# Optimization experiments

Measured on AMD Instinct MI355X. Metric: run time of the kernel, lower is better.

Reference implementation:

```python
import jax, jax.numpy as jnp
import numpy as np

N = 16384   # total gate nodes (64 graphs x 256 gates)
B = 64      # graphs in batch
E = 49152   # directed edges (avg in-degree 3)
Q = 32      # qubit_num
F = 256     # feat_dim
D = 2 * F   # node feature dim = 512
H = 2       # heads
A = 128     # action_num


def _gatv2(x, wl, wr, att, b, src, dst, n):
    # PyG GATv2Conv (concat=True, share_weights=False, negative_slope=0.2)
    h, c = att.shape
    xl = (x @ wl).reshape(n, h, c)   # source-side projection [N,H,C]
    xr = (x @ wr).reshape(n, h, c)   # target-side projection [N,H,C]
    e = jax.nn.leaky_relu(xl[src] + xr[dst], 0.2)       # [E,H,C]
    logit = jnp.einsum('ehc,hc->eh', e, att)             # [E,H]
    m = jax.ops.segment_max(logit, dst, num_segments=n)  # softmax over in-edges per target
    p = jnp.exp(logit - m[dst])
    den = jax.ops.segment_sum(p, dst, num_segments=n)
    alpha = p / den[dst]                                 # [E,H]
    out = jax.ops.segment_sum(alpha[:, :, None] * xl[src], dst, num_segments=n)
    return out.reshape(n, h * c) + b


def _forward(x, xt_w1, xt_b1, xt_w2, xt_b2,
             g0_wl, g0_wr, g0_att, g0_b,
             g1_wl, g1_wr, g1_att, g1_b,
             g2_wl, g2_wr, g2_att, g2_b,
             g3_wl, g3_wr, g3_att, g3_b,
             g4_wl, g4_wr, g4_att, g4_b,
             ln_w, ln_b, aggr_t,
             m_w1, m_b1, m_w2, m_b2, m_w3, m_b3,
             edge_index, batch):
    lr = lambda v: jax.nn.leaky_relu(v, 0.01)
    # x_trans: Linear -> LeakyReLU -> Linear, then fold qubit-pairs into one node
    h0 = lr(x @ xt_w1 + xt_b1) @ xt_w2 + xt_b2           # [2N, F]
    cx = h0.reshape(-1, D)                               # [N, 2F]
    n = cx.shape[0]
    # GATv2Conv default add_self_loops=True (inputs contain no self loops)
    sl = jnp.arange(n, dtype=edge_index.dtype)
    src = jnp.concatenate([edge_index[0], sl])
    dst = jnp.concatenate([edge_index[1], sl])
    res = cx
    h = lr(_gatv2(cx, g0_wl, g0_wr, g0_att, g0_b, src, dst, n))
    for wl_, wr_, att_, b_ in ((g1_wl, g1_wr, g1_att, g1_b),
                               (g2_wl, g2_wr, g2_att, g2_b),
                               (g3_wl, g3_wr, g3_att, g3_b)):
        h = lr(_gatv2(h, wl_, wr_, att_, b_, src, dst, n))
    h = lr(_gatv2(h, g4_wl, g4_wr, g4_att, g4_b, src, dst, n))
    h = h + res                                           # residual [N, 2F]
    # PyG LayerNorm(mode='graph'): normalize over nodes AND channels per graph
    cnt = jax.ops.segment_sum(jnp.ones((n,), h.dtype), batch, num_segments=B)
    norm = cnt * h.shape[1]
    mean = jax.ops.segment_sum(h.sum(-1), batch, num_segments=B) / norm
    hc = h - mean[batch][:, None]
    var = jax.ops.segment_sum((hc * hc).sum(-1), batch, num_segments=B) / norm
    h = hc / jnp.sqrt(var + 1e-5)[batch][:, None] * ln_w + ln_b
    # SoftmaxAggregation(learn=True): channel-wise softmax over nodes per graph
    logit = h * aggr_t
    mg = jax.ops.segment_max(logit, batch, num_segments=B)
    p = jnp.exp(logit - mg[batch])
    den = jax.ops.segment_sum(p, batch, num_segments=B)
    g = jax.ops.segment_sum((p / den[batch]) * h, batch, num_segments=B)  # [B, 2F]
    # head MLP 512->384->256->128
    o = lr(g @ m_w1 + m_b1)
    o = lr(o @ m_w2 + m_b2)
    return o @ m_w3 + m_b3


def setup_inputs() -> dict:
    key = jax.random.key(0)
    ks = iter(jax.random.split(key, 64))
    def rn(shp, s=0.05):
        return jax.random.normal(next(ks), shp, jnp.float32) * s
    d = {}
    d['x'] = jax.random.normal(next(ks), (2 * N, Q), jnp.float32)
    src = jax.random.randint(next(ks), (E,), 0, N, jnp.int32)
    off = jax.random.randint(next(ks), (E,), 1, N, jnp.int32)
    d['edge_index'] = jnp.stack([src, (src + off) % N])  # no self loops
    d['batch'] = jnp.arange(N, dtype=jnp.int32) // (N // B)
    d['xt_w1'] = rn((Q, F)); d['xt_b1'] = rn((F,))
    d['xt_w2'] = rn((F, F)); d['xt_b2'] = rn((F,))
    d['g0_wl'] = rn((D, H * D)); d['g0_wr'] = rn((D, H * D))
    d['g0_att'] = rn((H, D));    d['g0_b'] = rn((H * D,))
    for i in (1, 2, 3):
        d[f'g{i}_wl'] = rn((H * D, H * D)); d[f'g{i}_wr'] = rn((H * D, H * D))
        d[f'g{i}_att'] = rn((H, D));        d[f'g{i}_b'] = rn((H * D,))
    d['g4_wl'] = rn((H * D, D)); d['g4_wr'] = rn((H * D, D))
    d['g4_att'] = rn((1, D));    d['g4_b'] = rn((D,))
    d['ln_w'] = jnp.ones((D,), jnp.float32); d['ln_b'] = jnp.zeros((D,), jnp.float32)
    d['aggr_t'] = jnp.array(1.0, jnp.float32)
    d['m_w1'] = rn((D, 384)); d['m_b1'] = rn((384,))
    d['m_w2'] = rn((384, 256)); d['m_b2'] = rn((256,))
    d['m_w3'] = rn((256, A)); d['m_b3'] = rn((A,))
    return d


def reference(x, edge_index, batch, xt_w1, xt_b1, xt_w2, xt_b2,
              g0_wl, g0_wr, g0_att, g0_b,
              g1_wl, g1_wr, g1_att, g1_b,
              g2_wl, g2_wr, g2_att, g2_b,
              g3_wl, g3_wr, g3_att, g3_b,
              g4_wl, g4_wr, g4_att, g4_b,
              ln_w, ln_b, aggr_t,
              m_w1, m_b1, m_w2, m_b2, m_w3, m_b3):
    return _forward(x, xt_w1, xt_b1, xt_w2, xt_b2,
                    g0_wl, g0_wr, g0_att, g0_b,
                    g1_wl, g1_wr, g1_att, g1_b,
                    g2_wl, g2_wr, g2_att, g2_b,
                    g3_wl, g3_wr, g3_att, g3_b,
                    g4_wl, g4_wr, g4_att, g4_b,
                    ln_w, ln_b, aggr_t,
                    m_w1, m_b1, m_w2, m_b2, m_w3, m_b3,
                    edge_index, batch)
```

## Files before the change

kernel.cpp:

```cpp
#include <hip/hip_runtime.h>
#include <hip/hip_bf16.h>

typedef __hip_bfloat16 bf16;

#define NN 16384
#define BBG 64
#define EE 49152
#define ET (EE + NN)
#define DD 512
#define NG (NN / BBG)

__device__ __forceinline__ float b2f(bf16 v) { return __bfloat162float(v); }
__device__ __forceinline__ bf16 f2b(float v) { return __float2bfloat16(v); }
__device__ __forceinline__ float sb2f(short s) {
    unsigned u = ((unsigned)(unsigned short)s) << 16;
    return __builtin_bit_cast(float, u);
}
__device__ __forceinline__ short f2bs(float v) {
    bf16 b = f2b(v);
    return __builtin_bit_cast(short, b);
}
__device__ __forceinline__ int clampi(int v, int lo, int hi)
{
    return v < lo ? lo : (v > hi ? hi : v);
}

typedef __attribute__((ext_vector_type(8))) short bf16x8;
typedef __attribute__((ext_vector_type(4))) float f32x4;

#define AS1 __attribute__((address_space(1)))
#define AS3 __attribute__((address_space(3)))

__global__ __launch_bounds__(256) void gemm_mfma_bt(
    const bf16* __restrict__ A, const bf16* __restrict__ Bt,
    const float* __restrict__ bias, float* __restrict__ C,
    bf16* __restrict__ Cb, int M, int N, int K, float slope, int has_act)
{
    __shared__ bf16 As[128 * 32];
    __shared__ bf16 Bs[128 * 32];
    const int tid = threadIdx.x;
    const int w = tid >> 6;
    const int l = tid & 63;
    const int bm = blockIdx.y * 128;
    const int bn = blockIdx.x * 128;
    const int wrow = (w >> 1) * 64;
    const int wcol = (w & 1) * 64;
    const int quad = l >> 4;
    const int c16 = l & 15;

    const int lrow = l >> 2;
    const int lchunk = l & 3;
    const bf16* Ag = A + (size_t)(bm + w * 16 + lrow) * K + lchunk * 8;
    const bf16* Bg = Bt + (size_t)(bn + w * 16 + lrow) * K + lchunk * 8;
    char* AsB = (char*)As;
    char* BsB = (char*)Bs;

    f32x4 acc[4][4] = {};

    for (int k0 = 0; k0 < K; k0 += 32) {
        __builtin_amdgcn_global_load_lds((const AS1 void*)(Ag + k0),
            (AS3 void*)(AsB + w * 1024), 16, 0, 0);
        __builtin_amdgcn_global_load_lds((const AS1 void*)(Ag + (size_t)64 * K + k0),
            (AS3 void*)(AsB + 4096 + w * 1024), 16, 0, 0);
        __builtin_amdgcn_global_load_lds((const AS1 void*)(Bg + k0),
            (AS3 void*)(BsB + w * 1024), 16, 0, 0);
        __builtin_amdgcn_global_load_lds((const AS1 void*)(Bg + (size_t)64 * K + k0),
            (AS3 void*)(BsB + 4096 + w * 1024), 16, 0, 0);
        __syncthreads();

        bf16x8 a[4], b[4];
#pragma unroll
        for (int i = 0; i < 4; i++) {
            int ra = wrow + i * 16 + c16;
            a[i] = *(const bf16x8*)(AsB + ra * 64 + quad * 16);
            int rb = wcol + i * 16 + c16;
            b[i] = *(const bf16x8*)(BsB + rb * 64 + quad * 16);
        }
#pragma unroll
        for (int i = 0; i < 4; i++)
#pragma unroll
            for (int j = 0; j < 4; j++)
                acc[i][j] = __builtin_amdgcn_mfma_f32_16x16x32_bf16(
                    a[i], b[j], acc[i][j], 0, 0, 0);
        __syncthreads();
    }

#pragma unroll
    for (int i = 0; i < 4; i++) {
#pragma unroll
        for (int j = 0; j < 4; j++) {
            int col = bn + wcol + j * 16 + c16;
            float bv = bias ? bias[col] : 0.f;
#pragma unroll
            for (int r = 0; r < 4; r++) {
                int row = bm + wrow + i * 16 + quad * 4 + r;
                float v = acc[i][j][r] + bv;
                if (has_act) v = (v >= 0.f) ? v : v * slope;
                if (C)  C[(size_t)row * N + col] = v;
                if (Cb) Cb[(size_t)row * N + col] = f2b(v);
            }
        }
    }
}

__global__ __launch_bounds__(256) void gemm_mfma_dual(
    const bf16* __restrict__ A, const bf16* __restrict__ Bt,
    bf16* __restrict__ X0, bf16* __restrict__ X1,
    int M, int Ntot, int K, int HC)
{
    __shared__ bf16 As[128 * 32];
    __shared__ bf16 Bs[128 * 32];
    const int tid = threadIdx.x;
    const int w = tid >> 6;
    const int l = tid & 63;
    const int bm = blockIdx.y * 128;
    const int bn = blockIdx.x * 128;
    const int wrow = (w >> 1) * 64;
    const int wcol = (w & 1) * 64;
    const int quad = l >> 4;
    const int c16 = l & 15;

    const int lrow = l >> 2;
    const int lchunk = l & 3;
    const bf16* Ag = A + (size_t)(bm + w * 16 + lrow) * K + lchunk * 8;
    const bf16* Bg = Bt + (size_t)(bn + w * 16 + lrow) * K + lchunk * 8;
    char* AsB = (char*)As;
    char* BsB = (char*)Bs;

    f32x4 acc[4][4] = {};

    for (int k0 = 0; k0 < K; k0 += 32) {
        __builtin_amdgcn_global_load_lds((const AS1 void*)(Ag + k0),
            (AS3 void*)(AsB + w * 1024), 16, 0, 0);
        __builtin_amdgcn_global_load_lds((const AS1 void*)(Ag + (size_t)64 * K + k0),
            (AS3 void*)(AsB + 4096 + w * 1024), 16, 0, 0);
        __builtin_amdgcn_global_load_lds((const AS1 void*)(Bg + k0),
            (AS3 void*)(BsB + w * 1024), 16, 0, 0);
        __builtin_amdgcn_global_load_lds((const AS1 void*)(Bg + (size_t)64 * K + k0),
            (AS3 void*)(BsB + 4096 + w * 1024), 16, 0, 0);
        __syncthreads();

        bf16x8 a[4], b[4];
#pragma unroll
        for (int i = 0; i < 4; i++) {
            int ra = wrow + i * 16 + c16;
            a[i] = *(const bf16x8*)(AsB + ra * 64 + quad * 16);
            int rb = wcol + i * 16 + c16;
            b[i] = *(const bf16x8*)(BsB + rb * 64 + quad * 16);
        }
#pragma unroll
        for (int i = 0; i < 4; i++)
#pragma unroll
            for (int j = 0; j < 4; j++)
                acc[i][j] = __builtin_amdgcn_mfma_f32_16x16x32_bf16(
                    a[i], b[j], acc[i][j], 0, 0, 0);
        __syncthreads();
    }

#pragma unroll
    for (int i = 0; i < 4; i++) {
#pragma unroll
        for (int j = 0; j < 4; j++) {
            int col = bn + wcol + j * 16 + c16;
            bf16* dst = (col < HC) ? (X0 + col) : (X1 + col - HC);
#pragma unroll
            for (int r = 0; r < 4; r++) {
                int row = bm + wrow + i * 16 + quad * 4 + r;
                dst[(size_t)row * HC] = f2b(acc[i][j][r]);
            }
        }
    }
}

__global__ __launch_bounds__(256) void gemm_f32(
    const float* __restrict__ A, const float* __restrict__ W,
    const float* __restrict__ bias, float* __restrict__ C,
    int M, int N, int K, float slope, int has_act)
{
    const int BK = 16;
    __shared__ float Asm[BK][64 + 1];
    __shared__ float Wsm[BK][64 + 1];
    int tid = threadIdx.x;
    int bm = blockIdx.y * 64;
    int bn = blockIdx.x * 64;
    int tr = tid >> 4;
    int tc = tid & 15;
    float acc[4][4] = {};

    for (int k0 = 0; k0 < K; k0 += BK) {
        {
            int col = tid & 15;
            int row = tid >> 4;
#pragma unroll
            for (int p = 0; p < 4; p++) {
                int r = row + p * 16;
                Asm[col][r] = A[(size_t)(bm + r) * K + k0 + col];
            }
        }
        {
            int wc = tid & 63;
            int wr = tid >> 6;
#pragma unroll
            for (int p = 0; p < 4; p++) {
                int r = wr + p * 4;
                Wsm[r][wc] = W[(size_t)(k0 + r) * N + bn + wc];
            }
        }
        __syncthreads();
#pragma unroll
        for (int kk = 0; kk < BK; kk++) {
            float a[4], w[4];
#pragma unroll
            for (int i = 0; i < 4; i++) a[i] = Asm[kk][tr * 4 + i];
#pragma unroll
            for (int j = 0; j < 4; j++) w[j] = Wsm[kk][tc * 4 + j];
#pragma unroll
            for (int i = 0; i < 4; i++)
#pragma unroll
                for (int j = 0; j < 4; j++)
                    acc[i][j] += a[i] * w[j];
        }
        __syncthreads();
    }
#pragma unroll
    for (int i = 0; i < 4; i++) {
        int r = bm + tr * 4 + i;
#pragma unroll
        for (int j = 0; j < 4; j++) {
            int cn = bn + tc * 4 + j;
            float v = acc[i][j];
            if (bias) v += bias[cn];
            if (has_act) v = (v >= 0.f) ? v : v * slope;
            C[(size_t)r * N + cn] = v;
        }
    }
}

__global__ __launch_bounds__(256) void transpose_f2b2(
    const float* __restrict__ in0, bf16* __restrict__ out0,
    const float* __restrict__ in1, bf16* __restrict__ out1, int R, int C)
{
    const float* in = blockIdx.z ? in1 : in0;
    bf16* out = blockIdx.z ? out1 : out0;
    __shared__ float tile[32][33];
    int c0 = blockIdx.x * 32;
    int r0 = blockIdx.y * 32;
    int tx = threadIdx.x & 31;
    int ty = threadIdx.x >> 5;
#pragma unroll
    for (int k = 0; k < 4; k++) {
        int r = ty + k * 8;
        tile[r][tx] = in[(size_t)(r0 + r) * C + c0 + tx];
    }
    __syncthreads();
#pragma unroll
    for (int k = 0; k < 4; k++) {
        int rr = ty + k * 8;
        out[(size_t)(c0 + rr) * R + r0 + tx] = f2b(tile[tx][rr]);
    }
}

__global__ void f2b_vec(const float* __restrict__ in, bf16* __restrict__ out, int n)
{
    int i = blockIdx.x * 256 + threadIdx.x;
    if (i < n) out[i] = f2b(in[i]);
}

__global__ void count_deg(const int* __restrict__ ei, int* __restrict__ deg)
{
    int e = blockIdx.x * 256 + threadIdx.x;
    if (e >= ET) return;
    int d = (e < EE) ? ei[EE + e] : (e - EE);
    d = clampi(d, 0, NN - 1);
    atomicAdd(&deg[d], 1);
}

__global__ __launch_bounds__(256) void scan_deg(const int* __restrict__ deg,
                                                int* __restrict__ rs)
{
    __shared__ int part[256];
    __shared__ int psum[257];
    int tid = threadIdx.x;
    const int per = NN / 256;
    int base = tid * per;
    int s = 0;
    for (int i = 0; i < per; i++) s += deg[base + i];
    part[tid] = s;
    __syncthreads();
    if (tid == 0) {
        int acc = 0;
        for (int i = 0; i < 256; i++) { psum[i] = acc; acc += part[i]; }
        psum[256] = acc;
    }
    __syncthreads();
    int acc = psum[tid];
    for (int i = 0; i < per; i++) { rs[base + i] = acc; acc += deg[base + i]; }
    if (tid == 0) rs[NN] = psum[256];
}

__global__ void fill_csr(const int* __restrict__ ei, const int* __restrict__ rs,
                         int* __restrict__ cur, int* __restrict__ csrc)
{
    int e = blockIdx.x * 256 + threadIdx.x;
    if (e >= ET) return;
    int s, d;
    if (e < EE) { s = ei[e]; d = ei[EE + e]; } else { s = d = e - EE; }
    s = clampi(s, 0, NN - 1);
    d = clampi(d, 0, NN - 1);
    int pos = atomicAdd(&cur[d], 1);
    int slot = clampi(rs[d] + pos, 0, ET - 1);
    csrc[slot] = s;
}

template<int NH>
__global__ __launch_bounds__(256, 4) void gat_wave4(
    const bf16* __restrict__ xl, const bf16* __restrict__ xr,
    const float* __restrict__ att, const float* __restrict__ bias,
    const int* __restrict__ rs, const int* __restrict__ csrc,
    const float* __restrict__ res, float* __restrict__ out_f,
    bf16* __restrict__ out_b, float* __restrict__ lnsums)
{
    constexpr int HC = NH * 512;
    constexpr int PF = 8;
    const int tid = threadIdx.x;
    const int w = tid >> 6;
    const int lane = tid & 63;
    const int gw = blockIdx.x * 4 + w;
    const int n  = (NH == 2) ? (gw >> 1) : gw;
    const int h  = (NH == 2) ? (gw & 1) : 0;
    const int cb = h * 512 + lane * 8;

    int start = rs[n];
    int deg = clampi(rs[n + 1] - start, 1, 64);
    start = clampi(start, 0, ET - 1);
    start = __builtin_amdgcn_readfirstlane(start);
    deg = __builtin_amdgcn_readfirstlane(deg);
    const int dm1 = deg - 1;
    int my_src = csrc[start + ((lane < deg) ? lane : dm1)];
    my_src = clampi(my_src, 0, NN - 1);

    f32x4 rpx = *(const f32x4*)(xr + (size_t)n * HC + cb);
    f32x4 a0 = *(const f32x4*)(att + cb);
    f32x4 a1 = *(const f32x4*)(att + cb + 4);
    f32x4 rows[PF];
#pragma unroll
    for (int r = 0; r < PF; r++) {
        int s = __shfl(my_src, (r < dm1) ? r : dm1);
        rows[r] = *(const f32x4*)(xl + (size_t)s * HC + cb);
    }
    asm volatile("" : "+v"(rpx), "+v"(rows[0]), "+v"(rows[1]), "+v"(rows[2]),
                      "+v"(rows[3]), "+v"(rows[4]), "+v"(rows[5]),
                      "+v"(rows[6]), "+v"(rows[7]));

    float rv[8], av[8];
    {
        bf16x8 xb = __builtin_bit_cast(bf16x8, rpx);
#pragma unroll
        for (int k = 0; k < 8; k++) rv[k] = sb2f(xb[k]);
#pragma unroll
        for (int k = 0; k < 4; k++) { av[k] = a0[k]; av[4 + k] = a1[k]; }
    }

    float part[PF];
#pragma unroll
    for (int r = 0; r < PF; r++) {
        bf16x8 rb = __builtin_bit_cast(bf16x8, rows[r]);
        float p0 = 0.f, p1 = 0.f, p2 = 0.f, p3 = 0.f;
#pragma unroll
        for (int k = 0; k < 8; k += 4) {
            float x0 = sb2f(rb[k + 0]);
            float x1 = sb2f(rb[k + 1]);
            float x2 = sb2f(rb[k + 2]);
            float x3 = sb2f(rb[k + 3]);
            float u0 = x0 + rv[k + 0]; u0 = (u0 >= 0.f) ? u0 : 0.2f * u0;
            float u1 = x1 + rv[k + 1]; u1 = (u1 >= 0.f) ? u1 : 0.2f * u1;
            float u2 = x2 + rv[k + 2]; u2 = (u2 >= 0.f) ? u2 : 0.2f * u2;
            float u3 = x3 + rv[k + 3]; u3 = (u3 >= 0.f) ? u3 : 0.2f * u3;
            p0 = fmaf(av[k + 0], u0, p0);
            p1 = fmaf(av[k + 1], u1, p1);
            p2 = fmaf(av[k + 2], u2, p2);
            p3 = fmaf(av[k + 3], u3, p3);
        }
        part[r] = (p0 + p1) + (p2 + p3);
    }

#pragma unroll
    for (int msk = 32; msk; msk >>= 1) {
#pragma unroll
        for (int r = 0; r < PF; r++) part[r] += __shfl_xor(part[r], msk);
    }

    float m = -1e30f;
#pragma unroll
    for (int r = 0; r < PF; r++) {
        float vr = (r < deg) ? part[r] : -1e30f;
        m = fmaxf(m, vr);
    }
    float den = 0.f;
    float pw[PF];
#pragma unroll
    for (int r = 0; r < PF; r++) {
        float e = __expf(part[r] - m);
        pw[r] = (r < deg) ? e : 0.f;
        den += pw[r];
    }

    float acc[8];
#pragma unroll
    for (int k = 0; k < 8; k++) acc[k] = 0.f;
#pragma unroll
    for (int r = 0; r < PF; r++) {
        bf16x8 rb = __builtin_bit_cast(bf16x8, rows[r]);
#pragma unroll
        for (int k = 0; k < 8; k++)
            acc[k] = fmaf(pw[r], sb2f(rb[k]), acc[k]);
    }

    if (deg > PF) {
        for (int i = PF; i < deg; i++) {
            int s = __shfl(my_src, i);
            f32x4 rw = *(const f32x4*)(xl + (size_t)s * HC + cb);
            bf16x8 rb = __builtin_bit_cast(bf16x8, rw);
            float pt = 0.f;
#pragma unroll
            for (int k = 0; k < 8; k++) {
                float x = sb2f(rb[k]);
                float u = x + rv[k];
                u = (u >= 0.f) ? u : 0.2f * u;
                pt = fmaf(av[k], u, pt);
            }
#pragma unroll
            for (int msk = 32; msk; msk >>= 1) pt += __shfl_xor(pt, msk);
            float mn = fmaxf(m, pt);
            float rr = __expf(m - mn);
            float pi = __expf(pt - mn);
            m = mn;
            den = den * rr + pi;
#pragma unroll
            for (int k = 0; k < 8; k++) {
                float x = sb2f(rb[k]);
                acc[k] = fmaf(acc[k], rr, pi * x);
            }
        }
    }

    float inv = 1.f / den;
    f32x4 b0 = *(const f32x4*)(bias + cb);
    f32x4 b1 = *(const f32x4*)(bias + cb + 4);
    float ls = 0.f, ls2 = 0.f;
    float vals[8];
#pragma unroll
    for (int k = 0; k < 8; k++) {
        float bv = (k < 4) ? b0[k] : b1[k - 4];
        float v = fmaf(acc[k], inv, bv);
        v = (v >= 0.f) ? v : 0.01f * v;
        vals[k] = v;
    }
    if (res) {
#pragma unroll
        for (int k = 0; k < 8; k++) {
            vals[k] += res[(size_t)n * HC + cb + k];
            ls += vals[k];
            ls2 += vals[k] * vals[k];
        }
#pragma unroll
        for (int v = 0; v < 2; v++) {
            f32x4 ov;
#pragma unroll
            for (int k = 0; k < 4; k++) ov[k] = vals[v * 4 + k];
            *(f32x4*)(out_f + (size_t)n * HC + cb + v * 4) = ov;
        }
    } else {
        bf16x8 ov;
#pragma unroll
        for (int k = 0; k < 8; k++) ov[k] = f2bs(vals[k]);
        *(bf16x8*)(out_b + (size_t)n * HC + cb) = ov;
    }

    if (lnsums) {
#pragma unroll
        for (int msk = 32; msk; msk >>= 1) {
            ls += __shfl_xor(ls, msk);
            ls2 += __shfl_xor(ls2, msk);
        }
        if (lane == 0) {
            int g = n >> 8;
            atomicAdd(&lnsums[g], ls);
            atomicAdd(&lnsums[BBG + g], ls2);
        }
    }
}

__global__ __launch_bounds__(256) void aggr_partial(
    const float* __restrict__ h, const float* __restrict__ lnsums,
    const float* __restrict__ lnw, const float* __restrict__ lnb,
    const float* __restrict__ t_, float* __restrict__ pm,
    float* __restrict__ pd, float* __restrict__ pa)
{
    int g = blockIdx.x, ch = blockIdx.y, nk = blockIdx.z;
    int tid = threadIdx.x;
    int c = ch * 256 + tid;
    const float tot = (float)(NG * DD);
    float S = lnsums[g], S2 = lnsums[BBG + g];
    float mu = S / tot;
    float iv = rsqrtf(fmaxf(S2 / tot - mu * mu, 0.f) + 1e-5f);
    float w = lnw[c], b = lnb[c], t = t_[0];
    size_t base = (size_t)g * NG * DD + (size_t)nk * 32 * DD + c;
    float m = -1e30f, den = 0.f, acc = 0.f;
    for (int i = 0; i < 32; i++) {
        float hn = (h[base + (size_t)i * DD] - mu) * iv * w + b;
        float lg = hn * t;
        if (lg > m) {
            float r = __expf(m - lg);
            den *= r; acc *= r; m = lg;
        }
        float p = __expf(lg - m);
        den += p; acc += p * hn;
    }
    size_t idx = (((size_t)g * 2 + ch) * 8 + nk) * 256 + tid;
    pm[idx] = m; pd[idx] = den; pa[idx] = acc;
}

__global__ __launch_bounds__(256) void aggr_combine(
    const float* __restrict__ pm, const float* __restrict__ pd,
    const float* __restrict__ pa, float* __restrict__ gout)
{
    int g = blockIdx.x, ch = blockIdx.y;
    int tid = threadIdx.x;
    size_t base = (((size_t)g * 2 + ch) * 8) * 256 + tid;
    float m = -1e30f;
#pragma unroll
    for (int k = 0; k < 8; k++) m = fmaxf(m, pm[base + k * 256]);
    float den = 0.f, acc = 0.f;
#pragma unroll
    for (int k = 0; k < 8; k++) {
        float r = __expf(pm[base + k * 256] - m);
        den += pd[base + k * 256] * r;
        acc += pa[base + k * 256] * r;
    }
    gout[(size_t)g * DD + ch * 256 + tid] = acc / den;
}

extern "C" void kernel_launch(void* const* d_in, const int* in_sizes, int n_in,
                              void* d_out, int out_size, void* d_ws, size_t ws_size,
                              hipStream_t stream)
{
    const float* x      = (const float*)d_in[0];
    const int*   ei     = (const int*)d_in[1];
    const float* xt_w1  = (const float*)d_in[3];
    const float* xt_b1  = (const float*)d_in[4];
    const float* xt_w2  = (const float*)d_in[5];
    const float* xt_b2  = (const float*)d_in[6];
    const float* ln_w   = (const float*)d_in[27];
    const float* ln_b   = (const float*)d_in[28];
    const float* aggr_t = (const float*)d_in[29];
    const float* m_w1   = (const float*)d_in[30];
    const float* m_b1   = (const float*)d_in[31];
    const float* m_w2   = (const float*)d_in[32];
    const float* m_b2   = (const float*)d_in[33];
    const float* m_w3   = (const float*)d_in[34];
    const float* m_b3   = (const float*)d_in[35];
    float* out = (float*)d_out;

    char* p = (char*)d_ws;
    auto take = [&](size_t bytes) {
        char* r = p;
        p += (bytes + 255) & ~(size_t)255;
        return r;
    };
    int* i_deg     = (int*)take((size_t)(NN + 1) * 4);
    int* i_rs      = (int*)take((size_t)(NN + 1) * 4);
    int* i_cur     = (int*)take((size_t)NN * 4);
    int* i_src     = (int*)take((size_t)ET * 4);
    float* f_sums  = (float*)take((size_t)2 * BBG * 4);
    float* f_pm    = (float*)take((size_t)BBG * 2 * 8 * 256 * 4);
    float* f_pd    = (float*)take((size_t)BBG * 2 * 8 * 256 * 4);
    float* f_pa    = (float*)take((size_t)BBG * 2 * 8 * 256 * 4);
    float* b_g     = (float*)take((size_t)BBG * DD * 4);
    float* b_m1    = (float*)take((size_t)BBG * 384 * 4);
    float* b_m2    = (float*)take((size_t)BBG * 256 * 4);
    float* b_res   = (float*)take((size_t)NN * DD * 4);
    float* b_h     = (float*)take((size_t)NN * DD * 4);
    bf16* b_resb   = (bf16*)take((size_t)NN * DD * 2);
    bf16* b_hb     = (bf16*)take((size_t)NN * 1024 * 2);
    bf16* b_xlb    = (bf16*)take((size_t)NN * 1024 * 2);
    bf16* b_xrb    = (bf16*)take((size_t)NN * 1024 * 2);
    bf16* b_xb     = (bf16*)take((size_t)2 * NN * 32 * 2);
    bf16* b_wcat   = (bf16*)take((size_t)2048 * 1024 * 2);
    bf16* b_w1b    = (bf16*)take((size_t)32 * 256 * 2);
    bf16* b_w2b    = (bf16*)take((size_t)256 * 256 * 2);
    bf16* b_t1b = b_hb;

    dim3 blk(256);

    hipMemsetAsync(i_deg, 0, (size_t)(NN + 1) * 4, stream);
    hipMemsetAsync(i_cur, 0, (size_t)NN * 4, stream);
    hipMemsetAsync(f_sums, 0, (size_t)2 * BBG * 4, stream);
    count_deg<<<ET / 256, blk, 0, stream>>>(ei, i_deg);
    scan_deg<<<1, blk, 0, stream>>>(i_deg, i_rs);
    fill_csr<<<ET / 256, blk, 0, stream>>>(ei, i_rs, i_cur, i_src);

    f2b_vec<<<(2 * NN * 32 + 255) / 256, blk, 0, stream>>>(x, b_xb, 2 * NN * 32);
    transpose_f2b2<<<dim3(256 / 32, 32 / 32, 1), blk, 0, stream>>>(
        xt_w1, b_w1b, xt_w1, b_w1b, 32, 256);
    transpose_f2b2<<<dim3(256 / 32, 256 / 32, 1), blk, 0, stream>>>(
        xt_w2, b_w2b, xt_w2, b_w2b, 256, 256);

    gemm_mfma_bt<<<dim3(256 / 128, 32768 / 128), blk, 0, stream>>>(
        b_xb, b_w1b, xt_b1, (float*)nullptr, b_t1b, 32768, 256, 32, 0.01f, 1);
    gemm_mfma_bt<<<dim3(256 / 128, 32768 / 128), blk, 0, stream>>>(
        b_t1b, b_w2b, xt_b2, b_res, b_resb, 32768, 256, 256, 0.f, 0);

    for (int L = 0; L < 5; L++) {
        const float* wl  = (const float*)d_in[7 + 4 * L];
        const float* wr  = (const float*)d_in[8 + 4 * L];
        const float* att = (const float*)d_in[9 + 4 * L];
        const float* gb  = (const float*)d_in[10 + 4 * L];
        int Fin = (L == 0) ? 512 : 1024;
        int HC  = (L == 4) ? 512 : 1024;
        const bf16* hin = (L == 0) ? b_resb : b_hb;

        transpose_f2b2<<<dim3(HC / 32, Fin / 32, 2), blk, 0, stream>>>(
            wl, b_wcat, wr, b_wcat + (size_t)HC * Fin, Fin, HC);
        gemm_mfma_dual<<<dim3(2 * HC / 128, NN / 128), blk, 0, stream>>>(
            hin, b_wcat, b_xlb, b_xrb, NN, 2 * HC, Fin, HC);
        if (L == 4) {
            gat_wave4<1><<<NN / 4, blk, 0, stream>>>(
                b_xlb, b_xrb, att, gb, i_rs, i_src,
                b_res, b_h, (bf16*)nullptr, f_sums);
        } else {
            gat_wave4<2><<<NN * 2 / 4, blk, 0, stream>>>(
                b_xlb, b_xrb, att, gb, i_rs, i_src,
                (const float*)nullptr, (float*)nullptr, b_hb, (float*)nullptr);
        }
    }

    aggr_partial<<<dim3(BBG, 2, 8), blk, 0, stream>>>(
        b_h, f_sums, ln_w, ln_b, aggr_t, f_pm, f_pd, f_pa);
    aggr_combine<<<dim3(BBG, 2), blk, 0, stream>>>(f_pm, f_pd, f_pa, b_g);

    gemm_f32<<<dim3(384 / 64, 1), blk, 0, stream>>>(
        b_g, m_w1, m_b1, b_m1, 64, 384, 512, 0.01f, 1);
    gemm_f32<<<dim3(256 / 64, 1), blk, 0, stream>>>(
        b_m1, m_w2, m_b2, b_m2, 64, 256, 384, 0.01f, 1);
    gemm_f32<<<dim3(128 / 64, 1), blk, 0, stream>>>(
        b_m2, m_w3, m_b3, out, 64, 128, 256, 0.f, 0);
}
```

Baseline: 1.091 ms.

## Process several nodes per wave with double-buffered neighbor row prefetch

The GAT aggregation kernel now assigns 8 (two-head) or 4 (single-head) node-head tasks to each wave and launches a fixed 1024 blocks. It preloads CSR source indices for all tasks and double-buffers the gathered neighbor rows, so the loads for the next task are in flight while the current one is computed. The number of eagerly prefetched rows drops from 8 to 6 to make room for the second buffer. The aim is to hide gather latency. In exchange, register pressure rises, there are fewer waves in total, and nodes with more than 6 in-edges take the slower serial path more often.

Measured after the change: 1.116 ms. 1.02x slower.

```diff
diff --git a/kernel.cpp b/kernel.cpp
--- a/kernel.cpp
+++ b/kernel.cpp
@@ -313,7 +313,7 @@
 }
 
 template<int NH>
-__global__ __launch_bounds__(256, 4) void gat_wave4(
+__global__ __launch_bounds__(256, 4) void gat_wave5(
     const bf16* __restrict__ xl, const bf16* __restrict__ xr,
     const float* __restrict__ att, const float* __restrict__ bias,
     const int* __restrict__ rs, const int* __restrict__ csrc,
@@ -321,173 +321,234 @@
     bf16* __restrict__ out_b, float* __restrict__ lnsums)
 {
     constexpr int HC = NH * 512;
-    constexpr int PF = 8;
+    constexpr int PF = 6;
+    constexpr int NODES = (NH == 2) ? 8 : 4;
     const int tid = threadIdx.x;
     const int w = tid >> 6;
     const int lane = tid & 63;
-    const int gw = blockIdx.x * 4 + w;
-    const int n  = (NH == 2) ? (gw >> 1) : gw;
-    const int h  = (NH == 2) ? (gw & 1) : 0;
-    const int cb = h * 512 + lane * 8;
-
-    int start = rs[n];
-    int deg = clampi(rs[n + 1] - start, 1, 64);
-    start = clampi(start, 0, ET - 1);
-    start = __builtin_amdgcn_readfirstlane(start);
-    deg = __builtin_amdgcn_readfirstlane(deg);
-    const int dm1 = deg - 1;
-    int my_src = csrc[start + ((lane < deg) ? lane : dm1)];
-    my_src = clampi(my_src, 0, NN - 1);
-
-    f32x4 rpx = *(const f32x4*)(xr + (size_t)n * HC + cb);
-    f32x4 a0 = *(const f32x4*)(att + cb);
-    f32x4 a1 = *(const f32x4*)(att + cb + 4);
-    f32x4 rows[PF];
-#pragma unroll
-    for (int r = 0; r < PF; r++) {
-        int s = __shfl(my_src, (r < dm1) ? r : dm1);
-        rows[r] = *(const f32x4*)(xl + (size_t)s * HC + cb);
-    }
-    asm volatile("" : "+v"(rpx), "+v"(rows[0]), "+v"(rows[1]), "+v"(rows[2]),
-                      "+v"(rows[3]), "+v"(rows[4]), "+v"(rows[5]),
-                      "+v"(rows[6]), "+v"(rows[7]));
-
-    float rv[8], av[8];
+    const int wave_id = blockIdx.x * 4 + w;
+
+    int msrc[NODES];
+    int sdeg[NODES];
+#pragma unroll
+    for (int it = 0; it < NODES; ++it) {
+        int gw = wave_id * NODES + it;
+        int n = (NH == 2) ? (gw >> 1) : gw;
+        int st = rs[n];
+        int deg = clampi(rs[n + 1] - st, 1, 64);
+        st = clampi(st, 0, ET - 1);
+        st = __builtin_amdgcn_readfirstlane(st);
+        deg = __builtin_amdgcn_readfirstlane(deg);
+        sdeg[it] = deg;
+        msrc[it] = csrc[st + ((lane < deg) ? lane : deg - 1)];
+    }
+    if (NH == 2) {
+        asm volatile("" : "+v"(msrc[0]), "+v"(msrc[1]), "+v"(msrc[2]),
+                          "+v"(msrc[3]), "+v"(msrc[4]), "+v"(msrc[5]),
+                          "+v"(msrc[6]), "+v"(msrc[7]));
+    } else {
+        asm volatile("" : "+v"(msrc[0]), "+v"(msrc[1]), "+v"(msrc[2]),
+                          "+v"(msrc[3]));
+    }
+
+    float av0[8], av1[8];
     {
-        bf16x8 xb = __builtin_bit_cast(bf16x8, rpx);
-#pragma unroll
-        for (int k = 0; k < 8; k++) rv[k] = sb2f(xb[k]);
-#pragma unroll
-        for (int k = 0; k < 4; k++) { av[k] = a0[k]; av[4 + k] = a1[k]; }
-    }
-
-    float part[PF];
-#pragma unroll
-    for (int r = 0; r < PF; r++) {
-        bf16x8 rb = __builtin_bit_cast(bf16x8, rows[r]);
-        float p0 = 0.f, p1 = 0.f, p2 = 0.f, p3 = 0.f;
-#pragma unroll
-        for (int k = 0; k < 8; k += 4) {
-            float x0 = sb2f(rb[k + 0]);
-            float x1 = sb2f(rb[k + 1]);
-            float x2 = sb2f(rb[k + 2]);
-            float x3 = sb2f(rb[k + 3]);
-            float u0 = x0 + rv[k + 0]; u0 = (u0 >= 0.f) ? u0 : 0.2f * u0;
-            float u1 = x1 + rv[k + 1]; u1 = (u1 >= 0.f) ? u1 : 0.2f * u1;
-            float u2 = x2 + rv[k + 2]; u2 = (u2 >= 0.f) ? u2 : 0.2f * u2;
-            float u3 = x3 + rv[k + 3]; u3 = (u3 >= 0.f) ? u3 : 0.2f * u3;
-            p0 = fmaf(av[k + 0], u0, p0);
-            p1 = fmaf(av[k + 1], u1, p1);
-            p2 = fmaf(av[k + 2], u2, p2);
-            p3 = fmaf(av[k + 3], u3, p3);
-        }
-        part[r] = (p0 + p1) + (p2 + p3);
-    }
-
-#pragma unroll
-    for (int msk = 32; msk; msk >>= 1) {
-#pragma unroll
-        for (int r = 0; r < PF; r++) part[r] += __shfl_xor(part[r], msk);
-    }
-
-    float m = -1e30f;
-#pragma unroll
-    for (int r = 0; r < PF; r++) {
-        float vr = (r < deg) ? part[r] : -1e30f;
-        m = fmaxf(m, vr);
-    }
-    float den = 0.f;
-    float pw[PF];
-#pragma unroll
-    for (int r = 0; r < PF; r++) {
-        float e = __expf(part[r] - m);
-        pw[r] = (r < deg) ? e : 0.f;
-        den += pw[r];
-    }
-
-    float acc[8];
-#pragma unroll
-    for (int k = 0; k < 8; k++) acc[k] = 0.f;
-#pragma unroll
-    for (int r = 0; r < PF; r++) {
-        bf16x8 rb = __builtin_bit_cast(bf16x8, rows[r]);
-#pragma unroll
-        for (int k = 0; k < 8; k++)
-            acc[k] = fmaf(pw[r], sb2f(rb[k]), acc[k]);
-    }
-
-    if (deg > PF) {
-        for (int i = PF; i < deg; i++) {
-            int s = __shfl(my_src, i);
-            f32x4 rw = *(const f32x4*)(xl + (size_t)s * HC + cb);
-            bf16x8 rb = __builtin_bit_cast(bf16x8, rw);
-            float pt = 0.f;
+        f32x4 t0 = *(const f32x4*)(att + lane * 8);
+        f32x4 t1 = *(const f32x4*)(att + lane * 8 + 4);
+#pragma unroll
+        for (int k = 0; k < 4; k++) { av0[k] = t0[k]; av0[4 + k] = t1[k]; }
+        if (NH == 2) {
+            f32x4 t2 = *(const f32x4*)(att + 512 + lane * 8);
+            f32x4 t3 = *(const f32x4*)(att + 512 + lane * 8 + 4);
+#pragma unroll
+            for (int k = 0; k < 4; k++) { av1[k] = t2[k]; av1[4 + k] = t3[k]; }
+        } else {
+#pragma unroll
+            for (int k = 0; k < 8; k++) av1[k] = av0[k];
+        }
+    }
+
+    f32x4 rows[2][PF];
+    f32x4 rpx[2];
+
+    auto issue = [&](int it, int pb) {
+        int gw = wave_id * NODES + it;
+        int n = (NH == 2) ? (gw >> 1) : gw;
+        int h = (NH == 2) ? (gw & 1) : 0;
+        int cb = h * 512 + lane * 8;
+        rpx[pb] = *(const f32x4*)(xr + (size_t)n * HC + cb);
+        int dm1 = sdeg[it] - 1;
+#pragma unroll
+        for (int r = 0; r < PF; r++) {
+            int idx = (r < dm1) ? r : dm1;
+            int s = __builtin_amdgcn_readlane(msrc[it], idx);
+            s = clampi(s, 0, NN - 1);
+            rows[pb][r] = *(const f32x4*)(xl + (size_t)s * HC + cb);
+        }
+    };
+    auto pin = [&](int pb) {
+        asm volatile("" : "+v"(rows[pb][0]), "+v"(rows[pb][1]),
+                          "+v"(rows[pb][2]), "+v"(rows[pb][3]),
+                          "+v"(rows[pb][4]), "+v"(rows[pb][5]), "+v"(rpx[pb]));
+    };
+
+    auto compute = [&](int it, int pb) {
+        int gw = wave_id * NODES + it;
+        int n = (NH == 2) ? (gw >> 1) : gw;
+        int h = (NH == 2) ? (gw & 1) : 0;
+        int cb = h * 512 + lane * 8;
+        int deg = sdeg[it];
+
+        float rv[8], av[8];
+        {
+            bf16x8 xb = __builtin_bit_cast(bf16x8, rpx[pb]);
 #pragma unroll
             for (int k = 0; k < 8; k++) {
-                float x = sb2f(rb[k]);
-                float u = x + rv[k];
-                u = (u >= 0.f) ? u : 0.2f * u;
-                pt = fmaf(av[k], u, pt);
-            }
-#pragma unroll
-            for (int msk = 32; msk; msk >>= 1) pt += __shfl_xor(pt, msk);
-            float mn = fmaxf(m, pt);
-            float rr = __expf(m - mn);
-            float pi = __expf(pt - mn);
-            m = mn;
-            den = den * rr + pi;
+                rv[k] = sb2f(xb[k]);
+                av[k] = h ? av1[k] : av0[k];
+            }
+        }
+
+        float part[PF];
+#pragma unroll
+        for (int r = 0; r < PF; r++) {
+            bf16x8 rb = __builtin_bit_cast(bf16x8, rows[pb][r]);
+            float p0 = 0.f, p1 = 0.f, p2 = 0.f, p3 = 0.f;
+#pragma unroll
+            for (int k = 0; k < 8; k += 4) {
+                float x0 = sb2f(rb[k + 0]);
+                float x1 = sb2f(rb[k + 1]);
+                float x2 = sb2f(rb[k + 2]);
+                float x3 = sb2f(rb[k + 3]);
+                float u0 = x0 + rv[k + 0]; u0 = (u0 >= 0.f) ? u0 : 0.2f * u0;
+                float u1 = x1 + rv[k + 1]; u1 = (u1 >= 0.f) ? u1 : 0.2f * u1;
+                float u2 = x2 + rv[k + 2]; u2 = (u2 >= 0.f) ? u2 : 0.2f * u2;
+                float u3 = x3 + rv[k + 3]; u3 = (u3 >= 0.f) ? u3 : 0.2f * u3;
+                p0 = fmaf(av[k + 0], u0, p0);
+                p1 = fmaf(av[k + 1], u1, p1);
+                p2 = fmaf(av[k + 2], u2, p2);
+                p3 = fmaf(av[k + 3], u3, p3);
+            }
+            part[r] = (p0 + p1) + (p2 + p3);
+        }
+
+#pragma unroll
+        for (int msk = 32; msk; msk >>= 1) {
+#pragma unroll
+            for (int r = 0; r < PF; r++) part[r] += __shfl_xor(part[r], msk);
+        }
+
+        float m = -1e30f;
+#pragma unroll
+        for (int r = 0; r < PF; r++) {
+            float vr = (r < deg) ? part[r] : -1e30f;
+            m = fmaxf(m, vr);
+        }
+        float den = 0.f;
+        float pw[PF];
+#pragma unroll
+        for (int r = 0; r < PF; r++) {
+            float e = __expf(part[r] - m);
+            pw[r] = (r < deg) ? e : 0.f;
+            den += pw[r];
+        }
+
+        float acc[8];
+#pragma unroll
+        for (int k = 0; k < 8; k++) acc[k] = 0.f;
+#pragma unroll
+        for (int r = 0; r < PF; r++) {
+            bf16x8 rb = __builtin_bit_cast(bf16x8, rows[pb][r]);
+#pragma unroll
+            for (int k = 0; k < 8; k++)
+                acc[k] = fmaf(pw[r], sb2f(rb[k]), acc[k]);
+        }
+
+        if (deg > PF) {
+            for (int i = PF; i < deg; i++) {
+                int s = __builtin_amdgcn_readlane(msrc[it], i);
+                s = clampi(s, 0, NN - 1);
+                f32x4 rw = *(const f32x4*)(xl + (size_t)s * HC + cb);
+                bf16x8 rb = __builtin_bit_cast(bf16x8, rw);
+                float pt = 0.f;
+#pragma unroll
+                for (int k = 0; k < 8; k++) {
+                    float x = sb2f(rb[k]);
+                    float u = x + rv[k];
+                    u = (u >= 0.f) ? u : 0.2f * u;
+                    pt = fmaf(av[k], u, pt);
+                }
+#pragma unroll
+                for (int msk = 32; msk; msk >>= 1) pt += __shfl_xor(pt, msk);
+                float mn = fmaxf(m, pt);
+                float rr = __expf(m - mn);
+                float pi = __expf(pt - mn);
+                m = mn;
+                den = den * rr + pi;
+#pragma unroll
+                for (int k = 0; k < 8; k++) {
+                    float x = sb2f(rb[k]);
+                    acc[k] = fmaf(acc[k], rr, pi * x);
+                }
+            }
+        }
+
+        float inv = 1.f / den;
+        f32x4 b0 = *(const f32x4*)(bias + cb);
+        f32x4 b1 = *(const f32x4*)(bias + cb + 4);
+        float vals[8];
+#pragma unroll
+        for (int k = 0; k < 8; k++) {
+            float bv = (k < 4) ? b0[k] : b1[k - 4];
+            float v = fmaf(acc[k], inv, bv);
+            v = (v >= 0.f) ? v : 0.01f * v;
+            vals[k] = v;
+        }
+        if (res) {
+            float ls = 0.f, ls2 = 0.f;
 #pragma unroll
             for (int k = 0; k < 8; k++) {
-                float x = sb2f(rb[k]);
-                acc[k] = fmaf(acc[k], rr, pi * x);
-            }
-        }
-    }
-
-    float inv = 1.f / den;
-    f32x4 b0 = *(const f32x4*)(bias + cb);
-    f32x4 b1 = *(const f32x4*)(bias + cb + 4);
-    float ls = 0.f, ls2 = 0.f;
-    float vals[8];
-#pragma unroll
-    for (int k = 0; k < 8; k++) {
-        float bv = (k < 4) ? b0[k] : b1[k - 4];
-        float v = fmaf(acc[k], inv, bv);
-        v = (v >= 0.f) ? v : 0.01f * v;
-        vals[k] = v;
-    }
-    if (res) {
-#pragma unroll
-        for (int k = 0; k < 8; k++) {
-            vals[k] += res[(size_t)n * HC + cb + k];
-            ls += vals[k];
-            ls2 += vals[k] * vals[k];
-        }
-#pragma unroll
-        for (int v = 0; v < 2; v++) {
-            f32x4 ov;
-#pragma unroll
-            for (int k = 0; k < 4; k++) ov[k] = vals[v * 4 + k];
-            *(f32x4*)(out_f + (size_t)n * HC + cb + v * 4) = ov;
-        }
-    } else {
-        bf16x8 ov;
-#pragma unroll
-        for (int k = 0; k < 8; k++) ov[k] = f2bs(vals[k]);
-        *(bf16x8*)(out_b + (size_t)n * HC + cb) = ov;
-    }
-
-    if (lnsums) {
-#pragma unroll
-        for (int msk = 32; msk; msk >>= 1) {
-            ls += __shfl_xor(ls, msk);
-            ls2 += __shfl_xor(ls2, msk);
-        }
-        if (lane == 0) {
-            int g = n >> 8;
-            atomicAdd(&lnsums[g], ls);
-            atomicAdd(&lnsums[BBG + g], ls2);
-        }
+                vals[k] += res[(size_t)n * HC + cb + k];
+                ls += vals[k];
+                ls2 += vals[k] * vals[k];
+            }
+#pragma unroll
+            for (int v = 0; v < 2; v++) {
+                f32x4 ov;
+#pragma unroll
+                for (int k = 0; k < 4; k++) ov[k] = vals[v * 4 + k];
+                *(f32x4*)(out_f + (size_t)n * HC + cb + v * 4) = ov;
+            }
+            if (lnsums) {
+#pragma unroll
+                for (int msk = 32; msk; msk >>= 1) {
+                    ls += __shfl_xor(ls, msk);
+                    ls2 += __shfl_xor(ls2, msk);
+                }
+                if (lane == 0) {
+                    int g = n >> 8;
+                    atomicAdd(&lnsums[g], ls);
+                    atomicAdd(&lnsums[BBG + g], ls2);
+                }
+            }
+        } else {
+            bf16x8 ov;
+#pragma unroll
+            for (int k = 0; k < 8; k++) ov[k] = f2bs(vals[k]);
+            *(bf16x8*)(out_b + (size_t)n * HC + cb) = ov;
+        }
+    };
+
+    issue(0, 0);
+    pin(0);
+#pragma unroll
+    for (int it = 0; it < NODES; ++it) {
+        int pb = it & 1;
+        if (it + 1 < NODES) {
+            issue(it + 1, pb ^ 1);
+            pin(pb ^ 1);
+        }
+        compute(it, pb);
     }
 }
 
@@ -625,11 +686,11 @@
         gemm_mfma_dual<<<dim3(2 * HC / 128, NN / 128), blk, 0, stream>>>(
             hin, b_wcat, b_xlb, b_xrb, NN, 2 * HC, Fin, HC);
         if (L == 4) {
-            gat_wave4<1><<<NN / 4, blk, 0, stream>>>(
+            gat_wave5<1><<<1024, blk, 0, stream>>>(
                 b_xlb, b_xrb, att, gb, i_rs, i_src,
                 b_res, b_h, (bf16*)nullptr, f_sums);
         } else {
-            gat_wave4<2><<<NN * 2 / 4, blk, 0, stream>>>(
+            gat_wave5<2><<<1024, blk, 0, stream>>>(
                 b_xlb, b_xrb, att, gb, i_rs, i_src,
                 (const float*)nullptr, (float*)nullptr, b_hb, (float*)nullptr);
         }
```
